# Kernel tuning notes

Measured on AMD Instinct MI355X. Metric: run time of the kernel, lower is better.

Reference implementation:

```python
import jax, jax.numpy as jnp
import numpy as np


def setup_inputs() -> dict:
    key = jax.random.key(0)
    k1, k2, k3 = jax.random.split(key, 3)
    B, T, I, H = 32, 2048, 512, 512
    x = jax.random.normal(k1, (B, T, I), dtype=jnp.float32)
    W_x = jax.random.normal(k2, (3, I, H), dtype=jnp.float32) / np.sqrt(I)
    W_h = jax.random.normal(k3, (3, H, H), dtype=jnp.float32) / np.sqrt(H)
    bias = jnp.zeros((3, H), dtype=jnp.float32)
    return {"x": x, "W_x": W_x, "W_h": W_h, "bias": bias}


def reference(x, W_x, W_h, bias):
    # x: [B, T, I]; W_x: [3, I, H]; W_h: [3, H, H]; bias: [3, H]
    B, T, I = x.shape
    H = W_h.shape[-1]
    # Precompute input-side contributions for all gates/timesteps (batched GEMM):
    # gx: [T, 3, B, H] = x @ W_x[g] + bias[g]
    gx = jnp.einsum('bti,gih->tgbh', x, W_x) + bias[:, None, :]

    W_hz, W_hr, W_hh = W_h[0], W_h[1], W_h[2]

    def step(h_prev, gx_t):
        # gx_t: [3, B, H]
        z = jax.nn.sigmoid(gx_t[0] + h_prev @ W_hz)          # update gate
        r = jax.nn.sigmoid(gx_t[1] + h_prev @ W_hr)          # reset gate
        h_tilde = jnp.tanh(gx_t[2] + (r * h_prev) @ W_hh)    # candidate
        h_t = (1.0 - z) * h_prev + z * h_tilde
        return h_t, h_t

    h0 = jnp.zeros((B, H), dtype=x.dtype)
    h_last, outs = jax.lax.scan(step, h0, gx)  # outs: [T, B, H]
    output = jnp.transpose(outs, (1, 0, 2))    # [B, T, H]
    return output, h_last
```

## Files before the change

kernel.cpp:

```cpp
#include <hip/hip_runtime.h>
#include <stdint.h>
#include <stddef.h>


#define AGENT __HIP_MEMORY_SCOPE_AGENT

typedef _Float16 h2v __attribute__((ext_vector_type(2)));

__device__ __forceinline__ uint32_t pk2u(float a, float b) {
  h2v r; r[0] = (_Float16)a; r[1] = (_Float16)b;
  return __builtin_bit_cast(uint32_t, r);
}
__device__ __forceinline__ h2v bc2(uint32_t u) { return __builtin_bit_cast(h2v, u); }
__device__ __forceinline__ float dot2f(h2v a, h2v b, float c) {
#if __has_builtin(__builtin_amdgcn_fdot2)
  return __builtin_amdgcn_fdot2(a, b, c, false);
#else
  return fmaf((float)a[1], (float)b[1], fmaf((float)a[0], (float)b[0], c));
#endif
}

__device__ __forceinline__ float sigmoidf_(float x) { return 1.0f / (1.0f + __expf(-x)); }
__device__ __forceinline__ float tanhf_(float x) { return 1.0f - 2.0f / (1.0f + __expf(2.0f * x)); }

__device__ __forceinline__ uint64_t ald64(const uint64_t* p) {
  return __hip_atomic_load(p, __ATOMIC_RELAXED, AGENT);
}
__device__ __forceinline__ void ast64(uint64_t* p, uint64_t v) {
  __hip_atomic_store(p, v, __ATOMIC_RELAXED, AGENT);
}

__global__ __launch_bounds__(512, 2) void gru_fused_kernel(
    const float* __restrict__ x,
    const float* __restrict__ Wx,
    const float* __restrict__ Wh,
    const float* __restrict__ bias,
    float* __restrict__ out,
    uint64_t* __restrict__ Pbuf,
    uint64_t* __restrict__ zbuf) {
  __shared__ _Float16 h16[512];
  __shared__ _Float16 x16[512];
  __shared__ _Float16 rh16[64];

  const int T = threadIdx.x;
  const int bid = blockIdx.x;
  const int xcd = bid & 7, ii = bid >> 3;
  const int batch = xcd * 4 + (ii >> 3);
  const int slice = ii & 7;
  const int c = T >> 3, s = T & 7;
  const int jg = slice * 64 + c;

  uint32_t wz2[64], wr2[64], wh2[64];
  {
    const float* Whz = Wh;
    const float* Whr = Wh + 262144;
    const float* Wxz = Wx;
    const float* Wxr = Wx + 262144;
#pragma unroll
    for (int j = 0; j < 16; ++j) {
      int p = (j + 2 * s) & 15;
      int k = s * 64 + 4 * p;
#pragma unroll
      for (int q = 0; q < 2; ++q) {
        int kk = k + 2 * q;
        wz2[2 * j + q]      = pk2u(Whz[(size_t)kk * 512 + jg], Whz[(size_t)(kk + 1) * 512 + jg]);
        wr2[2 * j + q]      = pk2u(Whr[(size_t)kk * 512 + jg], Whr[(size_t)(kk + 1) * 512 + jg]);
        wz2[32 + 2 * j + q] = pk2u(Wxz[(size_t)kk * 512 + jg], Wxz[(size_t)(kk + 1) * 512 + jg]);
        wr2[32 + 2 * j + q] = pk2u(Wxr[(size_t)kk * 512 + jg], Wxr[(size_t)(kk + 1) * 512 + jg]);
      }
    }
    const float* Whh = Wh + 524288;
    const float* Wxh = Wx + 524288;
#pragma unroll
    for (int j = 0; j < 16; ++j) {
      int k = slice * 64 + 4 * j;
#pragma unroll
      for (int q = 0; q < 2; ++q) {
        int kk = k + 2 * q;
        wh2[2 * j + q]      = pk2u(Whh[(size_t)kk * 512 + T], Whh[(size_t)(kk + 1) * 512 + T]);
        wh2[32 + 2 * j + q] = pk2u(Wxh[(size_t)kk * 512 + T], Wxh[(size_t)(kk + 1) * 512 + T]);
      }
    }
  }
#pragma unroll
  for (int i = 0; i < 64; ++i) {
    asm volatile("" : "+v"(wz2[i]));
    asm volatile("" : "+v"(wr2[i]));
    asm volatile("" : "+v"(wh2[i]));
  }
  const float bz = bias[jg], br = bias[512 + jg], bh = bias[1024 + T];

  float hreg = 0.0f;
  h16[T] = (_Float16)0.0f;
  float x_p = x[((size_t)batch * 2048) * 512 + T];

  uint64_t* Pmine = Pbuf + ((size_t)batch * 8 + slice) * 512 + T;
  const uint64_t* Pread = Pbuf + ((size_t)batch * 8) * 512 + T;
  uint64_t* zmine = zbuf + (size_t)batch * 512 + jg;
  const uint64_t* zread = zbuf + (size_t)batch * 512 + T;

  for (int t = 0; t < 2048; ++t) {
    if (t > 0) {
      const size_t po = ((t - 1) & 1) ? 131072 : 0;
      const size_t zo = ((t - 1) & 1) ? 16384 : 0;
      const uint32_t want = (uint32_t)t;
      uint64_t v[8];
#pragma unroll
      for (int g = 0; g < 8; ++g) v[g] = ald64(Pread + po + (size_t)g * 512);
      uint64_t zv = ald64(zread + zo);
      for (;;) {
        bool ok = true;
        if ((uint32_t)(zv >> 32) != want) { zv = ald64(zread + zo); ok = false; }
#pragma unroll
        for (int g = 0; g < 8; ++g)
          if ((uint32_t)(v[g] >> 32) != want) { v[g] = ald64(Pread + po + (size_t)g * 512); ok = false; }
        if (ok) break;
        __builtin_amdgcn_s_sleep(1);
      }
      float hsum = 0.f;
#pragma unroll
      for (int g = 0; g < 8; ++g) hsum += __uint_as_float((uint32_t)v[g]);
      float zf = __uint_as_float((uint32_t)zv);
      float htil = tanhf_(bh + hsum);
      float hn = fmaf(zf, htil - hreg, hreg);
      if (slice == 0) out[((size_t)batch * 2048 + (t - 1)) * 512 + T] = hn;
      hreg = hn;
      h16[T] = (_Float16)hn;
    }
    x16[T] = (_Float16)x_p;
    __syncthreads();
    if (t < 2047) x_p = x[((size_t)batch * 2048 + t + 1) * 512 + T];

    float za = 0.f, ra = 0.f;
#pragma unroll
    for (int j = 0; j < 16; ++j) {
      int p = (j + 2 * s) & 15;
      int k = s * 64 + 4 * p;
      uint2 hu = *(const uint2*)&h16[k];
      uint2 xu = *(const uint2*)&x16[k];
      za = dot2f(bc2(hu.x), bc2(wz2[2 * j]), za);
      za = dot2f(bc2(hu.y), bc2(wz2[2 * j + 1]), za);
      ra = dot2f(bc2(hu.x), bc2(wr2[2 * j]), ra);
      ra = dot2f(bc2(hu.y), bc2(wr2[2 * j + 1]), ra);
      za = dot2f(bc2(xu.x), bc2(wz2[32 + 2 * j]), za);
      za = dot2f(bc2(xu.y), bc2(wz2[33 + 2 * j]), za);
      ra = dot2f(bc2(xu.x), bc2(wr2[32 + 2 * j]), ra);
      ra = dot2f(bc2(xu.y), bc2(wr2[33 + 2 * j]), ra);
    }
#pragma unroll
    for (int d = 1; d < 8; d <<= 1) { za += __shfl_xor(za, d); ra += __shfl_xor(ra, d); }
    const size_t po = (t & 1) ? 131072 : 0;
    const size_t zo = (t & 1) ? 16384 : 0;
    const uint64_t tagw = ((uint64_t)(uint32_t)(t + 1)) << 32;
    float z = sigmoidf_(za + bz);
    float r = sigmoidf_(ra + br);
    if (s == 0) {
      rh16[c] = (_Float16)(r * (float)h16[jg]);
      ast64(zmine + zo, tagw | (uint32_t)__float_as_uint(z));
    }
    __syncthreads();

    float pa = 0.f;
#pragma unroll
    for (int j = 0; j < 16; ++j) {
      uint2 ru = *(const uint2*)&rh16[4 * j];
      uint2 xu = *(const uint2*)&x16[slice * 64 + 4 * j];
      pa = dot2f(bc2(ru.x), bc2(wh2[2 * j]), pa);
      pa = dot2f(bc2(ru.y), bc2(wh2[2 * j + 1]), pa);
      pa = dot2f(bc2(xu.x), bc2(wh2[32 + 2 * j]), pa);
      pa = dot2f(bc2(xu.y), bc2(wh2[33 + 2 * j]), pa);
    }
    ast64(Pmine + po, tagw | (uint32_t)__float_as_uint(pa));
    __syncthreads();
  }

  {
    const uint32_t want = 2048u;
    uint64_t v[8];
#pragma unroll
    for (int g = 0; g < 8; ++g) v[g] = ald64(Pread + 131072 + (size_t)g * 512);
    uint64_t zv = ald64(zread + 16384);
    for (;;) {
      bool ok = true;
      if ((uint32_t)(zv >> 32) != want) { zv = ald64(zread + 16384); ok = false; }
#pragma unroll
      for (int g = 0; g < 8; ++g)
        if ((uint32_t)(v[g] >> 32) != want) { v[g] = ald64(Pread + 131072 + (size_t)g * 512); ok = false; }
      if (ok) break;
      __builtin_amdgcn_s_sleep(1);
    }
    float hsum = 0.f;
#pragma unroll
    for (int g = 0; g < 8; ++g) hsum += __uint_as_float((uint32_t)v[g]);
    float zf = __uint_as_float((uint32_t)zv);
    float htil = tanhf_(bh + hsum);
    float hn = fmaf(zf, htil - hreg, hreg);
    if (slice == 0) {
      out[((size_t)batch * 2048 + 2047) * 512 + T] = hn;
      out[(size_t)32 * 2048 * 512 + (size_t)batch * 512 + T] = hn;
    }
  }
}

extern "C" void kernel_launch(void* const* d_in, const int* in_sizes, int n_in,
                              void* d_out, int out_size, void* d_ws, size_t ws_size,
                              hipStream_t stream) {
  (void)in_sizes; (void)n_in; (void)out_size; (void)ws_size;
  const float* x    = (const float*)d_in[0];
  const float* Wx   = (const float*)d_in[1];
  const float* Wh   = (const float*)d_in[2];
  const float* bias = (const float*)d_in[3];
  float* out = (float*)d_out;
  char* ws = (char*)d_ws;

  uint64_t* Pbuf = (uint64_t*)ws;
  uint64_t* zbuf = (uint64_t*)(ws + 2097152);

  hipMemsetAsync(ws, 0, 2621440, stream);
  gru_fused_kernel<<<256, 512, 0, stream>>>(x, Wx, Wh, bias, out, Pbuf, zbuf);
}
```

Before: 8.631 ms.

## Precompute z/r input projections with an MFMA GEMM and split the scan across 1024 threads

A new fp16 MFMA GEMM kernel computes the input-side z and r gate pre-activations, with bias, for all timesteps up front. It stores them as fp16 in the output buffer, which the scan kernel then overwrites row by row after consuming them. The recurrent scan no longer does the x·W_x dot products for z/r on the serial critical path. It uses 1024 threads per block so each thread has a shorter reduction, and combines the candidate-gate halves through shared memory. The cost is an extra kernel launch and a pass over x, plus reliance on output-buffer aliasing that only holds because consumption stays ahead of the writes, and fp16 rounding of the gate inputs.

```diff
diff --git a/kernel.cpp b/kernel.cpp
--- a/kernel.cpp
+++ b/kernel.cpp
@@ -6,6 +6,8 @@
 #define AGENT __HIP_MEMORY_SCOPE_AGENT
 
 typedef _Float16 h2v __attribute__((ext_vector_type(2)));
+typedef _Float16 half8 __attribute__((ext_vector_type(8)));
+typedef float f32x4 __attribute__((ext_vector_type(4)));
 
 __device__ __forceinline__ uint32_t pk2u(float a, float b) {
   h2v r; r[0] = (_Float16)a; r[1] = (_Float16)b;
@@ -19,10 +21,8 @@
   return fmaf((float)a[1], (float)b[1], fmaf((float)a[0], (float)b[0], c));
 #endif
 }
-
 __device__ __forceinline__ float sigmoidf_(float x) { return 1.0f / (1.0f + __expf(-x)); }
 __device__ __forceinline__ float tanhf_(float x) { return 1.0f - 2.0f / (1.0f + __expf(2.0f * x)); }
-
 __device__ __forceinline__ uint64_t ald64(const uint64_t* p) {
   return __hip_atomic_load(p, __ATOMIC_RELAXED, AGENT);
 }
@@ -30,74 +30,157 @@
   __hip_atomic_store(p, v, __ATOMIC_RELAXED, AGENT);
 }
 
-__global__ __launch_bounds__(512, 2) void gru_fused_kernel(
+__global__ __launch_bounds__(256) void gemm_gzr(const float* __restrict__ x,
+                                                const float* __restrict__ Wx,
+                                                const float* __restrict__ bias,
+                                                _Float16* __restrict__ gzr) {
+  __shared__ alignas(16) _Float16 Alds[128 * 68];
+  __shared__ alignas(16) _Float16 Blds[128 * 68];
+  const int tid = threadIdx.x;
+  const int bid = blockIdx.x;
+  const int tm = bid >> 3, tn = bid & 7;
+  const int m0 = tm << 7, n0 = tn << 7;
+  const int lane = tid & 63;
+  const int wv = tid >> 6, wm = wv >> 1, wn = wv & 1;
+  const int l15 = lane & 15, lhi = lane >> 4;
+  f32x4 acc[4][4] = {};
+
+  for (int k0 = 0; k0 < 512; k0 += 64) {
+#pragma unroll
+    for (int r = 0; r < 8; ++r) {
+      int m = r * 16 + (tid >> 4);
+      int k = (tid & 15) * 4;
+      float4 v = *(const float4*)&x[(size_t)(m0 + m) * 512 + k0 + k];
+      union { _Float16 h[4]; uint2 u; } cv;
+      cv.h[0] = (_Float16)v.x; cv.h[1] = (_Float16)v.y;
+      cv.h[2] = (_Float16)v.z; cv.h[3] = (_Float16)v.w;
+      *(uint2*)&Alds[m * 68 + k] = cv.u;
+    }
+#pragma unroll
+    for (int u = 0; u < 8; ++u) {
+      int n = tid & 127;
+      int k = (tid >> 7) * 32 + u * 4;
+      int ng = n0 + n;
+      const float* wp = Wx + ((size_t)(ng >> 9) << 18) + (size_t)(k0 + k) * 512 + (ng & 511);
+      union { _Float16 h[4]; uint2 u2; } cv;
+      cv.h[0] = (_Float16)wp[0];    cv.h[1] = (_Float16)wp[512];
+      cv.h[2] = (_Float16)wp[1024]; cv.h[3] = (_Float16)wp[1536];
+      *(uint2*)&Blds[n * 68 + k] = cv.u2;
+    }
+    __syncthreads();
+#pragma unroll
+    for (int kk = 0; kk < 2; ++kk) {
+      int q = kk * 4 + lhi;
+      half8 af[4], bf[4];
+#pragma unroll
+      for (int fm = 0; fm < 4; ++fm) {
+        const _Float16* pa = &Alds[(wm * 64 + fm * 16 + l15) * 68 + q * 8];
+        union { uint2 u[2]; half8 h; } cv;
+        cv.u[0] = *(const uint2*)pa; cv.u[1] = *(const uint2*)(pa + 4);
+        af[fm] = cv.h;
+      }
+#pragma unroll
+      for (int fn = 0; fn < 4; ++fn) {
+        const _Float16* pb = &Blds[(wn * 64 + fn * 16 + l15) * 68 + q * 8];
+        union { uint2 u[2]; half8 h; } cv;
+        cv.u[0] = *(const uint2*)pb; cv.u[1] = *(const uint2*)(pb + 4);
+        bf[fn] = cv.h;
+      }
+#pragma unroll
+      for (int fm = 0; fm < 4; ++fm)
+#pragma unroll
+        for (int fn = 0; fn < 4; ++fn)
+          acc[fm][fn] = __builtin_amdgcn_mfma_f32_16x16x32_f16(af[fm], bf[fn], acc[fm][fn], 0, 0, 0);
+    }
+    __syncthreads();
+  }
+#pragma unroll
+  for (int fn = 0; fn < 4; ++fn) {
+    int col = n0 + wn * 64 + fn * 16 + l15;
+    float bv = bias[((col >> 9) << 9) + (col & 511)];
+#pragma unroll
+    for (int fm = 0; fm < 4; ++fm) {
+#pragma unroll
+      for (int q2 = 0; q2 < 4; ++q2) {
+        int row = m0 + wm * 64 + fm * 16 + lhi * 4 + q2;
+        gzr[(size_t)row * 1024 + col] = (_Float16)(acc[fm][fn][q2] + bv);
+      }
+    }
+  }
+}
+
+__global__ __launch_bounds__(1024) void gru_scan(
     const float* __restrict__ x,
     const float* __restrict__ Wx,
     const float* __restrict__ Wh,
     const float* __restrict__ bias,
-    float* __restrict__ out,
+    const _Float16* gzr,
+    float* out,
     uint64_t* __restrict__ Pbuf,
     uint64_t* __restrict__ zbuf) {
   __shared__ _Float16 h16[512];
-  __shared__ _Float16 x16[512];
+  __shared__ _Float16 x16s[64];
   __shared__ _Float16 rh16[64];
+  __shared__ float Pparts[2][512];
 
   const int T = threadIdx.x;
   const int bid = blockIdx.x;
   const int xcd = bid & 7, ii = bid >> 3;
   const int batch = xcd * 4 + (ii >> 3);
   const int slice = ii & 7;
-  const int c = T >> 3, s = T & 7;
+  const int c = T >> 4, s = T & 15;
   const int jg = slice * 64 + c;
-
-  uint32_t wz2[64], wr2[64], wh2[64];
+  const int n = T & 511, half = T >> 9;
+
+  uint32_t wz2[16], wr2[16], wh2[16], wx2[16];
   {
     const float* Whz = Wh;
     const float* Whr = Wh + 262144;
-    const float* Wxz = Wx;
-    const float* Wxr = Wx + 262144;
-#pragma unroll
-    for (int j = 0; j < 16; ++j) {
-      int p = (j + 2 * s) & 15;
-      int k = s * 64 + 4 * p;
+#pragma unroll
+    for (int j = 0; j < 8; ++j) {
+      int p = (j + s) & 7;
+      int k = s * 32 + 4 * p;
 #pragma unroll
       for (int q = 0; q < 2; ++q) {
         int kk = k + 2 * q;
-        wz2[2 * j + q]      = pk2u(Whz[(size_t)kk * 512 + jg], Whz[(size_t)(kk + 1) * 512 + jg]);
-        wr2[2 * j + q]      = pk2u(Whr[(size_t)kk * 512 + jg], Whr[(size_t)(kk + 1) * 512 + jg]);
-        wz2[32 + 2 * j + q] = pk2u(Wxz[(size_t)kk * 512 + jg], Wxz[(size_t)(kk + 1) * 512 + jg]);
-        wr2[32 + 2 * j + q] = pk2u(Wxr[(size_t)kk * 512 + jg], Wxr[(size_t)(kk + 1) * 512 + jg]);
+        wz2[2 * j + q] = pk2u(Whz[(size_t)kk * 512 + jg], Whz[(size_t)(kk + 1) * 512 + jg]);
+        wr2[2 * j + q] = pk2u(Whr[(size_t)kk * 512 + jg], Whr[(size_t)(kk + 1) * 512 + jg]);
       }
     }
     const float* Whh = Wh + 524288;
     const float* Wxh = Wx + 524288;
 #pragma unroll
-    for (int j = 0; j < 16; ++j) {
-      int k = slice * 64 + 4 * j;
+    for (int j = 0; j < 8; ++j) {
+      int k = slice * 64 + half * 32 + 4 * j;
 #pragma unroll
       for (int q = 0; q < 2; ++q) {
         int kk = k + 2 * q;
-        wh2[2 * j + q]      = pk2u(Whh[(size_t)kk * 512 + T], Whh[(size_t)(kk + 1) * 512 + T]);
-        wh2[32 + 2 * j + q] = pk2u(Wxh[(size_t)kk * 512 + T], Wxh[(size_t)(kk + 1) * 512 + T]);
-      }
-    }
-  }
-#pragma unroll
-  for (int i = 0; i < 64; ++i) {
+        wh2[2 * j + q] = pk2u(Whh[(size_t)kk * 512 + n], Whh[(size_t)(kk + 1) * 512 + n]);
+        wx2[2 * j + q] = pk2u(Wxh[(size_t)kk * 512 + n], Wxh[(size_t)(kk + 1) * 512 + n]);
+      }
+    }
+  }
+#pragma unroll
+  for (int i = 0; i < 16; ++i) {
     asm volatile("" : "+v"(wz2[i]));
     asm volatile("" : "+v"(wr2[i]));
     asm volatile("" : "+v"(wh2[i]));
-  }
-  const float bz = bias[jg], br = bias[512 + jg], bh = bias[1024 + T];
+    asm volatile("" : "+v"(wx2[i]));
+  }
+  const float bh = bias[1024 + n];
 
   float hreg = 0.0f;
-  h16[T] = (_Float16)0.0f;
-  float x_p = x[((size_t)batch * 2048) * 512 + T];
-
-  uint64_t* Pmine = Pbuf + ((size_t)batch * 8 + slice) * 512 + T;
-  const uint64_t* Pread = Pbuf + ((size_t)batch * 8) * 512 + T;
+  if (half == 0) h16[n] = (_Float16)0.0f;
+
+  const size_t rowbase = (size_t)batch * 2048;
+  _Float16 gz_p = gzr[rowbase * 1024 + jg];
+  _Float16 gr_p = gzr[rowbase * 1024 + 512 + jg];
+  float x_p = (T < 64) ? x[rowbase * 512 + slice * 64 + T] : 0.f;
+
+  uint64_t* Pmine = Pbuf + ((size_t)batch * 8 + slice) * 512 + n;
+  const uint64_t* Pread = Pbuf + ((size_t)batch * 8) * 512 + n;
   uint64_t* zmine = zbuf + (size_t)batch * 512 + jg;
-  const uint64_t* zread = zbuf + (size_t)batch * 512 + T;
+  const uint64_t* zread = zbuf + (size_t)batch * 512 + n;
 
   for (int t = 0; t < 2048; ++t) {
     if (t > 0) {
@@ -123,37 +206,38 @@
       float zf = __uint_as_float((uint32_t)zv);
       float htil = tanhf_(bh + hsum);
       float hn = fmaf(zf, htil - hreg, hreg);
-      if (slice == 0) out[((size_t)batch * 2048 + (t - 1)) * 512 + T] = hn;
+      if (slice == 0 && half == 0) out[(rowbase + (t - 1)) * 512 + n] = hn;
       hreg = hn;
-      h16[T] = (_Float16)hn;
-    }
-    x16[T] = (_Float16)x_p;
-    __syncthreads();
-    if (t < 2047) x_p = x[((size_t)batch * 2048 + t + 1) * 512 + T];
+      if (half == 0) h16[n] = (_Float16)hn;
+    }
+    float gzc = (float)gz_p, grc = (float)gr_p;
+    if (T < 64) x16s[T] = (_Float16)x_p;
+    __syncthreads();
+    if (t < 2047) {
+      size_t r1 = rowbase + t + 1;
+      gz_p = gzr[r1 * 1024 + jg];
+      gr_p = gzr[r1 * 1024 + 512 + jg];
+      if (T < 64) x_p = x[r1 * 512 + slice * 64 + T];
+    }
 
     float za = 0.f, ra = 0.f;
 #pragma unroll
-    for (int j = 0; j < 16; ++j) {
-      int p = (j + 2 * s) & 15;
-      int k = s * 64 + 4 * p;
+    for (int j = 0; j < 8; ++j) {
+      int p = (j + s) & 7;
+      int k = s * 32 + 4 * p;
       uint2 hu = *(const uint2*)&h16[k];
-      uint2 xu = *(const uint2*)&x16[k];
       za = dot2f(bc2(hu.x), bc2(wz2[2 * j]), za);
       za = dot2f(bc2(hu.y), bc2(wz2[2 * j + 1]), za);
       ra = dot2f(bc2(hu.x), bc2(wr2[2 * j]), ra);
       ra = dot2f(bc2(hu.y), bc2(wr2[2 * j + 1]), ra);
-      za = dot2f(bc2(xu.x), bc2(wz2[32 + 2 * j]), za);
-      za = dot2f(bc2(xu.y), bc2(wz2[33 + 2 * j]), za);
-      ra = dot2f(bc2(xu.x), bc2(wr2[32 + 2 * j]), ra);
-      ra = dot2f(bc2(xu.y), bc2(wr2[33 + 2 * j]), ra);
-    }
-#pragma unroll
-    for (int d = 1; d < 8; d <<= 1) { za += __shfl_xor(za, d); ra += __shfl_xor(ra, d); }
+    }
+#pragma unroll
+    for (int d = 1; d < 16; d <<= 1) { za += __shfl_xor(za, d); ra += __shfl_xor(ra, d); }
     const size_t po = (t & 1) ? 131072 : 0;
     const size_t zo = (t & 1) ? 16384 : 0;
     const uint64_t tagw = ((uint64_t)(uint32_t)(t + 1)) << 32;
-    float z = sigmoidf_(za + bz);
-    float r = sigmoidf_(ra + br);
+    float z = sigmoidf_(za + gzc);
+    float r = sigmoidf_(ra + grc);
     if (s == 0) {
       rh16[c] = (_Float16)(r * (float)h16[jg]);
       ast64(zmine + zo, tagw | (uint32_t)__float_as_uint(z));
@@ -162,16 +246,20 @@
 
     float pa = 0.f;
 #pragma unroll
-    for (int j = 0; j < 16; ++j) {
-      uint2 ru = *(const uint2*)&rh16[4 * j];
-      uint2 xu = *(const uint2*)&x16[slice * 64 + 4 * j];
+    for (int j = 0; j < 8; ++j) {
+      uint2 ru = *(const uint2*)&rh16[half * 32 + 4 * j];
+      uint2 xu = *(const uint2*)&x16s[half * 32 + 4 * j];
       pa = dot2f(bc2(ru.x), bc2(wh2[2 * j]), pa);
       pa = dot2f(bc2(ru.y), bc2(wh2[2 * j + 1]), pa);
-      pa = dot2f(bc2(xu.x), bc2(wh2[32 + 2 * j]), pa);
-      pa = dot2f(bc2(xu.y), bc2(wh2[33 + 2 * j]), pa);
-    }
-    ast64(Pmine + po, tagw | (uint32_t)__float_as_uint(pa));
-    __syncthreads();
+      pa = dot2f(bc2(xu.x), bc2(wx2[2 * j]), pa);
+      pa = dot2f(bc2(xu.y), bc2(wx2[2 * j + 1]), pa);
+    }
+    Pparts[half][n] = pa;
+    __syncthreads();
+    if (half == 0) {
+      float ps = Pparts[0][n] + Pparts[1][n];
+      ast64(Pmine + po, tagw | (uint32_t)__float_as_uint(ps));
+    }
   }
 
   {
@@ -195,9 +283,9 @@
     float zf = __uint_as_float((uint32_t)zv);
     float htil = tanhf_(bh + hsum);
     float hn = fmaf(zf, htil - hreg, hreg);
-    if (slice == 0) {
-      out[((size_t)batch * 2048 + 2047) * 512 + T] = hn;
-      out[(size_t)32 * 2048 * 512 + (size_t)batch * 512 + T] = hn;
+    if (slice == 0 && half == 0) {
+      out[(rowbase + 2047) * 512 + n] = hn;
+      out[(size_t)32 * 2048 * 512 + (size_t)batch * 512 + n] = hn;
     }
   }
 }
@@ -217,5 +305,7 @@
   uint64_t* zbuf = (uint64_t*)(ws + 2097152);
 
   hipMemsetAsync(ws, 0, 2621440, stream);
-  gru_fused_kernel<<<256, 512, 0, stream>>>(x, Wx, Wh, bias, out, Pbuf, zbuf);
-}
+  gemm_gzr<<<4096, 256, 0, stream>>>(x, Wx, bias, (_Float16*)d_out);
+  gru_scan<<<256, 1024, 0, stream>>>(x, Wx, Wh, bias, (const _Float16*)d_out,
+                                     out, Pbuf, zbuf);
+}
```

Result: slower. 10.91 ms (+26.5%).
